# Kernel tuning notes

Hardware: AMD Instinct MI355X
Metric: run time of the kernel (lower is better)

Reference implementation:

```python
import jax, jax.numpy as jnp
import numpy as np

B = 65536            # batch of configurations
F = 32               # num_frames (joints)
DOF = 29             # controllable joints
# tree: chain 0..29, two mimic branches off frame 10; parent index always < child -> topo order = range(F)
PARENTS = [-1] + list(range(29)) + [10, 10]


def _np_rodrigues(w):
    th = np.linalg.norm(w)
    if th < 1e-12:
        return np.eye(3)
    k = w / th
    K = np.array([[0, -k[2], k[1]], [k[2], 0, -k[0]], [-k[1], k[0], 0]])
    return np.eye(3) + np.sin(th) * K + (1 - np.cos(th)) * (K @ K)


def setup_inputs() -> dict:
    key = jax.random.key(0)
    rng = np.random.default_rng(0)
    # joint types: 0 fixed, 1 revolute, 2 prismatic
    types = np.ones(F, dtype=np.int32)
    types[0] = 0
    types[15] = 2
    types[22] = 2
    # controllable = non-fixed, non-mimic (mimic dst = 30, 31)
    ctrl = np.array([i for i in range(F) if types[i] != 0 and i not in (30, 31)], dtype=np.int32)
    assert ctrl.shape[0] == DOF
    axes = rng.normal(size=(F, 3)).astype(np.float32)
    axes /= np.linalg.norm(axes, axis=-1, keepdims=True)
    origins = np.tile(np.eye(4, dtype=np.float32), (F, 1, 1))
    for i in range(F):
        origins[i, :3, :3] = _np_rodrigues(rng.normal(size=3) * 0.5)
        origins[i, :3, 3] = rng.normal(size=3) * 0.1
    joint_angles = jax.random.normal(key, (B, DOF), dtype=jnp.float32)
    return {
        "joint_angles": joint_angles,
        "all_axes": jnp.asarray(axes),
        "all_origins": jnp.asarray(origins),
        "mimic_multipliers": jnp.array([1.0, -1.0], dtype=jnp.float32),
        "mimic_offsets": jnp.array([0.1, -0.1], dtype=jnp.float32),
        "ctrlable_indices": jnp.asarray(ctrl),
        "mimic_src_indices": jnp.array([5, 6], dtype=jnp.int32),
        "mimic_dst_indices": jnp.array([30, 31], dtype=jnp.int32),
        "joint_types": jnp.asarray(types),
    }


def exp_map(w):
    # axis-angle (...,3) -> rotation (...,3,3), Rodrigues, eps-safe at w=0
    theta = jnp.sqrt(jnp.sum(w * w, axis=-1, keepdims=True) + 1e-18)  # (...,1)
    k = w / theta
    kx, ky, kz = k[..., 0], k[..., 1], k[..., 2]
    zero = jnp.zeros_like(kx)
    K = jnp.stack(
        [jnp.stack([zero, -kz, ky], -1),
         jnp.stack([kz, zero, -kx], -1),
         jnp.stack([-ky, kx, zero], -1)], -2)
    st = jnp.sin(theta)[..., None]
    ct = jnp.cos(theta)[..., None]
    return jnp.eye(3, dtype=w.dtype) + st * K + (1.0 - ct) * (K @ K)


def _fk(joint_angles, all_axes, all_origins, mimic_multipliers, mimic_offsets,
        ctrlable_indices, mimic_src_indices, mimic_dst_indices, joint_types):
    b = joint_angles.shape[0]
    # scatter controllable angles, then mimic gather/scatter
    all_angles = jnp.zeros((b, F), joint_angles.dtype).at[:, ctrlable_indices].set(joint_angles)
    mimic_vals = all_angles[:, mimic_src_indices] * mimic_multipliers + mimic_offsets
    all_angles = all_angles.at[:, mimic_dst_indices].set(mimic_vals)
    # per-frame local motion (B,F,4,4)
    w = all_axes[None, :, :] * all_angles[..., None]          # (B,F,3)
    R = exp_map(w)                                            # (B,F,3,3)
    R = jnp.where((joint_types == 1)[None, :, None, None], R, jnp.eye(3, dtype=w.dtype))
    t = jnp.where((joint_types == 2)[None, :, None], w, jnp.zeros((), w.dtype))
    top = jnp.concatenate([R, t[..., None]], axis=-1)         # (B,F,3,4)
    bottom = jnp.broadcast_to(jnp.array([0, 0, 0, 1], w.dtype), (b, F, 1, 4))
    motion = jnp.concatenate([top, bottom], axis=-2)          # (B,F,4,4)
    local = jnp.einsum('fij,bfjk->bfik', all_origins, motion)
    # sequential tree-structured compose (F is small & static -> unrolled)
    poses = []
    for i in range(F):
        p = PARENTS[i]
        li = local[:, i]
        poses.append(li if p < 0 else poses[p] @ li)
    return jnp.stack(poses, axis=1)                            # (B,F,4,4)


def reference(joint_angles, all_axes, all_origins, mimic_multipliers, mimic_offsets,
              ctrlable_indices, mimic_src_indices, mimic_dst_indices, joint_types):
    return _fk(joint_angles, all_axes, all_origins, mimic_multipliers, mimic_offsets,
               ctrlable_indices, mimic_src_indices, mimic_dst_indices, joint_types)
```

## Files before the change

kernel.cpp:

```cpp
#include <hip/hip_runtime.h>
#include <math.h>

#define NF 32
#define NDOF 29
#define BLOCK 256
#define SLOT_DW 20

__device__ __forceinline__ void amul(float* __restrict__ N,
                                     const float* __restrict__ A,
                                     const float* __restrict__ B) {
    #pragma unroll
    for (int r = 0; r < 3; ++r) {
        const float a0 = A[r*4+0], a1 = A[r*4+1], a2 = A[r*4+2], a3 = A[r*4+3];
        N[r*4+0] = a0*B[0] + a1*B[4] + a2*B[8];
        N[r*4+1] = a0*B[1] + a1*B[5] + a2*B[9];
        N[r*4+2] = a0*B[2] + a1*B[6] + a2*B[10];
        N[r*4+3] = a0*B[3] + a1*B[7] + a2*B[11] + a3;
    }
}

__global__ __launch_bounds__(BLOCK) void fk_kernel(
    const float* __restrict__ ja,
    const float* __restrict__ axes,
    const float* __restrict__ origins,
    const float* __restrict__ mmul,
    const float* __restrict__ moff,
    const int*   __restrict__ ctrl,
    const int*   __restrict__ msrc,
    const int*   __restrict__ mdst,
    const int*   __restrict__ types,
    float*       __restrict__ out,
    int B)
{
    __shared__ float s_ax[NF][3];
    __shared__ float s_or[NF][12];
    __shared__ int   s_type[NF];
    __shared__ int   s_slot[NF];
    __shared__ float s_mult[NF];
    __shared__ float s_off[NF];
    __shared__ float s_stage[4][64 * SLOT_DW];

    const int tid  = threadIdx.x;
    const int lane = tid & 63;
    const int wv   = tid >> 6;
    const int sub  = lane & 7;
    const int grp  = lane & ~7;

    if (tid < NF) {
        const int f = tid;
        s_ax[f][0] = axes[f*3+0];
        s_ax[f][1] = axes[f*3+1];
        s_ax[f][2] = axes[f*3+2];
        #pragma unroll
        for (int i = 0; i < 12; ++i) s_or[f][i] = origins[f*16 + i];
        s_type[f] = types[f];
        int slot = -1;
        for (int j = 0; j < NDOF; ++j) if (ctrl[j] == f) slot = j;
        float mu = 1.0f, of = 0.0f;
        for (int m = 0; m < 2; ++m) {
            if (mdst[m] == f) {
                const int sf = msrc[m];
                for (int j = 0; j < NDOF; ++j) if (ctrl[j] == sf) slot = j;
                mu = mmul[m]; of = moff[m];
            }
        }
        s_slot[f] = slot; s_mult[f] = mu; s_off[f] = of;
    }
    __syncthreads();

    const long bat = (long)blockIdx.x * 32 + (tid >> 3);
    const bool bok = bat < (long)B;

    float M[4][12];
    #pragma unroll
    for (int j = 0; j < 4; ++j) {
        const int f    = 4*sub + j;
        const int slot = s_slot[f];
        float a = 0.0f;
        if (slot >= 0 && bok) a = fmaf(s_mult[f], ja[bat * NDOF + slot], s_off[f]);
        const float wx = a * s_ax[f][0];
        const float wy = a * s_ax[f][1];
        const float wz = a * s_ax[f][2];
        const int ty = s_type[f];
        float R0,R1,R2,R3,R4,R5,R6,R7,R8;
        if (ty == 1) {
            const float t2 = wx*wx + wy*wy + wz*wz;
            const float th = sqrtf(t2 + 1e-18f);
            const float inv = 1.0f / th;
            const float kx = wx*inv, ky = wy*inv, kz = wz*inv;
            float s, c;
            __sincosf(th, &s, &c);
            const float v = 1.0f - c;
            R0 = fmaf(v*kx, kx, c);
            R1 = v*kx*ky - s*kz;
            R2 = v*kx*kz + s*ky;
            R3 = v*kx*ky + s*kz;
            R4 = fmaf(v*ky, ky, c);
            R5 = v*ky*kz - s*kx;
            R6 = v*kx*kz - s*ky;
            R7 = v*ky*kz + s*kx;
            R8 = fmaf(v*kz, kz, c);
        } else {
            R0=1.f;R1=0.f;R2=0.f;R3=0.f;R4=1.f;R5=0.f;R6=0.f;R7=0.f;R8=1.f;
        }
        const float tx  = (ty == 2) ? wx : 0.0f;
        const float tyv = (ty == 2) ? wy : 0.0f;
        const float tz  = (ty == 2) ? wz : 0.0f;
        const float* O = s_or[f];
        #pragma unroll
        for (int r = 0; r < 3; ++r) {
            const float o0 = O[r*4+0], o1 = O[r*4+1], o2 = O[r*4+2], o3 = O[r*4+3];
            M[j][r*4+0] = o0*R0 + o1*R3 + o2*R6;
            M[j][r*4+1] = o0*R1 + o1*R4 + o2*R7;
            M[j][r*4+2] = o0*R2 + o1*R5 + o2*R8;
            M[j][r*4+3] = o0*tx + o1*tyv + o2*tz + o3;
        }
    }

    float I[12];
    #pragma unroll
    for (int i = 0; i < 12; ++i) I[i] = M[0][i];
    #pragma unroll
    for (int j = 1; j < 4; ++j) {
        float N[12];
        amul(N, I, M[j]);
        const bool keep = !(sub == 7 && j >= 2);
        #pragma unroll
        for (int i = 0; i < 12; ++i) I[i] = keep ? N[i] : I[i];
    }

    #pragma unroll
    for (int d = 1; d <= 4; d <<= 1) {
        const int src = grp | ((sub - d) & 7);
        float T[12];
        #pragma unroll
        for (int i = 0; i < 12; ++i) T[i] = __shfl(I[i], src, 64);
        float N[12];
        amul(N, T, I);
        const bool use = (sub >= d);
        #pragma unroll
        for (int i = 0; i < 12; ++i) I[i] = use ? N[i] : I[i];
    }

    const float ID[12] = {1,0,0,0, 0,1,0,0, 0,0,1,0};
    float run[12];
    {
        const int src = grp | ((sub - 1) & 7);
        #pragma unroll
        for (int i = 0; i < 12; ++i) {
            const float t = __shfl(I[i], src, 64);
            run[i] = (sub > 0) ? t : ID[i];
        }
    }

    float P10[12];
    #pragma unroll
    for (int i = 0; i < 12; ++i) P10[i] = run[i];
    #pragma unroll
    for (int j = 0; j < 4; ++j) {
        float N[12];
        amul(N, run, M[j]);
        const bool chain = !(sub == 7 && j >= 2);
        #pragma unroll
        for (int i = 0; i < 12; ++i) {
            M[j][i] = chain ? N[i] : M[j][i];
            run[i]  = chain ? N[i] : run[i];
        }
        if (j == 2 && sub == 2) {
            #pragma unroll
            for (int i = 0; i < 12; ++i) P10[i] = N[i];
        }
    }
    #pragma unroll
    for (int i = 0; i < 12; ++i) P10[i] = __shfl(P10[i], grp | 2, 64);
    #pragma unroll
    for (int j = 2; j < 4; ++j) {
        float N[12];
        amul(N, P10, M[j]);
        #pragma unroll
        for (int i = 0; i < 12; ++i) M[j][i] = (sub == 7) ? N[i] : M[j][i];
    }

    float* const st = s_stage[wv];
    const long wbat0 = (long)blockIdx.x * 32 + wv * 8;
    float4* const out4 = (float4*)out;
    const int row = lane & 3;

    #pragma unroll
    for (int j = 0; j < 4; ++j) {
        float4* wp = (float4*)&st[lane * SLOT_DW];
        wp[0] = make_float4(M[j][0], M[j][1], M[j][2],  M[j][3]);
        wp[1] = make_float4(M[j][4], M[j][5], M[j][6],  M[j][7]);
        wp[2] = make_float4(M[j][8], M[j][9], M[j][10], M[j][11]);
        wp[3] = make_float4(0.0f, 0.0f, 0.0f, 1.0f);
        __builtin_amdgcn_wave_barrier();
        #pragma unroll
        for (int m = 0; m < 4; ++m) {
            const int  slot = m * 16 + (lane >> 2);
            const float4 v  = *(const float4*)&st[slot * SLOT_DW + row * 4];
            const long bb   = wbat0 + (slot >> 3);
            const int  fr   = 4 * (slot & 7) + j;
            if (bb < (long)B)
                out4[bb * 128 + fr * 4 + row] = v;
        }
        __builtin_amdgcn_wave_barrier();
    }
}

extern "C" void kernel_launch(void* const* d_in, const int* in_sizes, int n_in,
                              void* d_out, int out_size, void* d_ws, size_t ws_size,
                              hipStream_t stream) {
    const float* ja   = (const float*)d_in[0];
    const float* axes = (const float*)d_in[1];
    const float* orig = (const float*)d_in[2];
    const float* mmul = (const float*)d_in[3];
    const float* moff = (const float*)d_in[4];
    const int*   ctrl = (const int*)d_in[5];
    const int*   msrc = (const int*)d_in[6];
    const int*   mdst = (const int*)d_in[7];
    const int*   typs = (const int*)d_in[8];
    float* out = (float*)d_out;

    const int B = in_sizes[0] / NDOF;
    const int grid = (B + 31) / 32;
    fk_kernel<<<grid, BLOCK, 0, stream>>>(ja, axes, orig, mmul, moff,
                                          ctrl, msrc, mdst, typs, out, B);
}
```

Baseline: 164.0 us.

## Stage joint angles in LDS, use DPP/swizzle scans, nontemporal output stores

The block's joint angles are now loaded into shared memory with one coalesced cooperative read, replacing strided per-thread global loads. The prefix-scan shuffles become DPP row_shr moves, and the P10 broadcast becomes a ds_swizzle, which avoids bpermute LDS traffic. Output float4 stores become nontemporal, and the launch bounds request 4 blocks per CU as an occupancy hint. The trade-off is an extra block-wide barrier to reuse the staging buffer, plus reliance on DPP and swizzle lane patterns that are only correct because each group is 8 lanes.

```diff
diff --git a/kernel.cpp b/kernel.cpp
--- a/kernel.cpp
+++ b/kernel.cpp
@@ -5,6 +5,8 @@
 #define NDOF 29
 #define BLOCK 256
 #define SLOT_DW 20
+
+typedef float fx4 __attribute__((ext_vector_type(4)));
 
 __device__ __forceinline__ void amul(float* __restrict__ N,
                                      const float* __restrict__ A,
@@ -19,7 +21,11 @@
     }
 }
 
-__global__ __launch_bounds__(BLOCK) void fk_kernel(
+#define DPP_SHR(dst, srcv, CTRL)                                              \
+    dst = __int_as_float(__builtin_amdgcn_update_dpp(                          \
+        0, __float_as_int(srcv), (CTRL), 0xF, 0xF, true))
+
+__global__ __launch_bounds__(BLOCK, 4) void fk_kernel(
     const float* __restrict__ ja,
     const float* __restrict__ axes,
     const float* __restrict__ origins,
@@ -39,12 +45,25 @@
     __shared__ float s_mult[NF];
     __shared__ float s_off[NF];
     __shared__ float s_stage[4][64 * SLOT_DW];
+    float* const s_ja = &s_stage[0][0];
 
     const int tid  = threadIdx.x;
     const int lane = tid & 63;
     const int wv   = tid >> 6;
     const int sub  = lane & 7;
-    const int grp  = lane & ~7;
+
+    {
+        const long jb   = (long)blockIdx.x * (32 * NDOF);
+        const long jtot = (long)B * NDOF;
+        #pragma unroll
+        for (int i = 0; i < 4; ++i) {
+            const int k = tid + i * BLOCK;
+            if (k < 32 * NDOF) {
+                const long g = jb + k;
+                s_ja[k] = (g < jtot) ? ja[g] : 0.0f;
+            }
+        }
+    }
 
     if (tid < NF) {
         const int f = tid;
@@ -68,8 +87,10 @@
     }
     __syncthreads();
 
-    const long bat = (long)blockIdx.x * 32 + (tid >> 3);
-    const bool bok = bat < (long)B;
+    const int  batl = tid >> 3;
+    const long bat  = (long)blockIdx.x * 32 + batl;
+    const bool bok  = bat < (long)B;
+    (void)bok;
 
     float M[4][12];
     #pragma unroll
@@ -77,7 +98,7 @@
         const int f    = 4*sub + j;
         const int slot = s_slot[f];
         float a = 0.0f;
-        if (slot >= 0 && bok) a = fmaf(s_mult[f], ja[bat * NDOF + slot], s_off[f]);
+        if (slot >= 0) a = fmaf(s_mult[f], s_ja[batl * NDOF + slot], s_off[f]);
         const float wx = a * s_ax[f][0];
         const float wy = a * s_ax[f][1];
         const float wz = a * s_ax[f][2];
@@ -116,6 +137,7 @@
             M[j][r*4+3] = o0*tx + o1*tyv + o2*tz + o3;
         }
     }
+    __syncthreads();
 
     float I[12];
     #pragma unroll
@@ -129,28 +151,28 @@
         for (int i = 0; i < 12; ++i) I[i] = keep ? N[i] : I[i];
     }
 
-    #pragma unroll
-    for (int d = 1; d <= 4; d <<= 1) {
-        const int src = grp | ((sub - d) & 7);
-        float T[12];
-        #pragma unroll
-        for (int i = 0; i < 12; ++i) T[i] = __shfl(I[i], src, 64);
-        float N[12];
-        amul(N, T, I);
-        const bool use = (sub >= d);
-        #pragma unroll
-        for (int i = 0; i < 12; ++i) I[i] = use ? N[i] : I[i];
-    }
-
-    const float ID[12] = {1,0,0,0, 0,1,0,0, 0,0,1,0};
+    #define SCAN_STEP(D, CTRL)                                                \
+    {                                                                         \
+        float T[12], Nn[12];                                                  \
+        _Pragma("unroll")                                                     \
+        for (int i = 0; i < 12; ++i) DPP_SHR(T[i], I[i], CTRL);               \
+        amul(Nn, T, I);                                                       \
+        const bool use = (sub >= (D));                                        \
+        _Pragma("unroll")                                                     \
+        for (int i = 0; i < 12; ++i) I[i] = use ? Nn[i] : I[i];               \
+    }
+    SCAN_STEP(1, 0x111)
+    SCAN_STEP(2, 0x112)
+    SCAN_STEP(4, 0x114)
+    #undef SCAN_STEP
+
     float run[12];
-    {
-        const int src = grp | ((sub - 1) & 7);
-        #pragma unroll
-        for (int i = 0; i < 12; ++i) {
-            const float t = __shfl(I[i], src, 64);
-            run[i] = (sub > 0) ? t : ID[i];
-        }
+    #pragma unroll
+    for (int i = 0; i < 12; ++i) {
+        float t;
+        DPP_SHR(t, I[i], 0x111);
+        const float idv = (i == 0 || i == 5 || i == 10) ? 1.0f : 0.0f;
+        run[i] = (sub > 0) ? t : idv;
     }
 
     float P10[12];
@@ -172,7 +194,9 @@
         }
     }
     #pragma unroll
-    for (int i = 0; i < 12; ++i) P10[i] = __shfl(P10[i], grp | 2, 64);
+    for (int i = 0; i < 12; ++i)
+        P10[i] = __int_as_float(
+            __builtin_amdgcn_ds_swizzle(__float_as_int(P10[i]), 0x58));
     #pragma unroll
     for (int j = 2; j < 4; ++j) {
         float N[12];
@@ -183,7 +207,7 @@
 
     float* const st = s_stage[wv];
     const long wbat0 = (long)blockIdx.x * 32 + wv * 8;
-    float4* const out4 = (float4*)out;
+    fx4* const out4 = (fx4*)out;
     const int row = lane & 3;
 
     #pragma unroll
@@ -197,11 +221,11 @@
         #pragma unroll
         for (int m = 0; m < 4; ++m) {
             const int  slot = m * 16 + (lane >> 2);
-            const float4 v  = *(const float4*)&st[slot * SLOT_DW + row * 4];
+            const fx4  v    = *(const fx4*)&st[slot * SLOT_DW + row * 4];
             const long bb   = wbat0 + (slot >> 3);
             const int  fr   = 4 * (slot & 7) + j;
             if (bb < (long)B)
-                out4[bb * 128 + fr * 4 + row] = v;
+                __builtin_nontemporal_store(v, &out4[bb * 128 + fr * 4 + row]);
         }
         __builtin_amdgcn_wave_barrier();
     }
```

Result: slower. 178.0 us (+8.6%).
